# Kernel optimization log

Hardware: AMD Instinct MI355X
Metric: run time of the kernel (lower is better)

Reference implementation:

```python
import jax, jax.numpy as jnp
import numpy as np

BATCH, TAU, INPUT, HIDDEN, OUT = 131072, 20, 1, 64, 1


def setup_inputs() -> dict:
    key = jax.random.key(0)
    ks = jax.random.split(key, 8)
    fan_in = INPUT + HIDDEN
    bound = 1.0 / np.sqrt(fan_in)
    return {
        "x": jax.random.normal(ks[0], (BATCH, TAU), dtype=jnp.float32),
        "h0": jax.random.normal(ks[1], (BATCH, HIDDEN), dtype=jnp.float32),
        "Wf": jax.random.uniform(ks[2], (HIDDEN, fan_in), jnp.float32, -bound, bound),
        "bf": jax.random.uniform(ks[3], (HIDDEN,), jnp.float32, -bound, bound),
        "Wc": jax.random.uniform(ks[4], (HIDDEN, fan_in), jnp.float32, -bound, bound),
        "bc": jax.random.uniform(ks[5], (HIDDEN,), jnp.float32, -bound, bound),
        "Wo": jax.random.uniform(ks[6], (OUT, HIDDEN), jnp.float32, -1.0 / np.sqrt(HIDDEN), 1.0 / np.sqrt(HIDDEN)),
        "bo": jax.random.uniform(ks[7], (OUT,), jnp.float32, -1.0 / np.sqrt(HIDDEN), 1.0 / np.sqrt(HIDDEN)),
    }


def reference(x, h0, Wf, bf, Wc, bc, Wo, bo):
    # x: [B, tau] -> xs: [tau, B, 1], matching torch.reshape(x.T, (tau, B, 1))
    xs = jnp.transpose(x)[:, :, None]

    def step(H, X):
        inp = jnp.concatenate([X, H], axis=1)              # [B, 1+H]
        F = jax.nn.sigmoid(inp @ Wf.T + bf)                # forget gate [B, H]
        inp2 = jnp.concatenate([X, F * H], axis=1)
        H_tilda = jnp.tanh(inp2 @ Wc.T + bc)               # candidate [B, H]
        H_new = (1.0 - F) * H + F * H_tilda
        return H_new, None

    H, _ = jax.lax.scan(step, h0, xs)
    return H @ Wo.T + bo                                   # [B, 1]
```

## Files before the change

kernel.cpp:

```cpp
#include <hip/hip_runtime.h>


constexpr int BATCH = 131072;
constexpr int TAU   = 20;
constexpr int HID   = 64;
constexpr int FAN   = 65;
constexpr int NT    = 256;
constexpr int ROWS  = 64;

typedef float    f32x4 __attribute__((ext_vector_type(4)));
typedef _Float16 f16x8 __attribute__((ext_vector_type(8)));
typedef unsigned u32x4 __attribute__((ext_vector_type(4)));

static constexpr float LOG2E  = 1.4426950408889634f;
static constexpr float RCP256 = 0.00390625f;

static __device__ __forceinline__ unsigned pkrtz(float a, float b) {
    return __builtin_bit_cast(unsigned, __builtin_amdgcn_cvt_pkrtz(a, b));
}
#define PK8(a0,a1,a2,a3,a4,a5,a6,a7) \
    __builtin_bit_cast(f16x8, (u32x4){pkrtz(a0,a1), pkrtz(a2,a3), \
                                      pkrtz(a4,a5), pkrtz(a6,a7)})

#define MFMAH(A, B, C) __builtin_amdgcn_mfma_f32_16x16x32_f16((A), (B), (C), 0, 0, 0)

#define HOFF(g, T, s) ((((g) * 8) + ((T) * 2) + (s)) * 512)

#define LD_HI(g, T, s)  (*(const f16x8*)&sWhi[HOFF(g, T, s) + Lx8])
#define LD_AUG(g, T)    (*(const f16x8*)&sAug[augMul * ((g) * 4 + (T)) + augSel])

#define SIGF4(F, C) { \
    const float e0_ = __builtin_amdgcn_exp2f(C[0]); \
    const float e1_ = __builtin_amdgcn_exp2f(C[1]); \
    const float e2_ = __builtin_amdgcn_exp2f(C[2]); \
    const float e3_ = __builtin_amdgcn_exp2f(C[3]); \
    const float d0_ = 1.0f + e0_, d1_ = 1.0f + e1_; \
    const float d2_ = 1.0f + e2_, d3_ = 1.0f + e3_; \
    const float d01_ = d0_ * d1_, d23_ = d2_ * d3_; \
    const float ii_  = __builtin_amdgcn_rcpf(d01_ * d23_); \
    const float i01_ = ii_ * d23_, i23_ = ii_ * d01_; \
    F[0] = d1_ * i01_; F[1] = d0_ * i01_; \
    F[2] = d3_ * i23_; F[3] = d2_ * i23_; }

#define UPDF4(S, F, C) { \
    const float e0_ = __builtin_amdgcn_exp2f(C[0]); \
    const float e1_ = __builtin_amdgcn_exp2f(C[1]); \
    const float e2_ = __builtin_amdgcn_exp2f(C[2]); \
    const float e3_ = __builtin_amdgcn_exp2f(C[3]); \
    const float d0_ = 1.0f + e0_, d1_ = 1.0f + e1_; \
    const float d2_ = 1.0f + e2_, d3_ = 1.0f + e3_; \
    const float d01_ = d0_ * d1_, d23_ = d2_ * d3_; \
    const float ii_  = __builtin_amdgcn_rcpf(d01_ * d23_); \
    const float j01_ = -2.0f * (ii_ * d23_), j23_ = -2.0f * (ii_ * d01_); \
    const float t0_ = fmaf(d1_, j01_, 1.0f); \
    const float t1_ = fmaf(d0_, j01_, 1.0f); \
    const float t2_ = fmaf(d3_, j23_, 1.0f); \
    const float t3_ = fmaf(d2_, j23_, 1.0f); \
    S[0] = fmaf(F[0], t0_ - S[0], S[0]); S[1] = fmaf(F[1], t1_ - S[1], S[1]); \
    S[2] = fmaf(F[2], t2_ - S[2], S[2]); S[3] = fmaf(F[3], t3_ - S[3], S[3]); }

#define FTILE(T, FT) { \
    f32x4 ch_ = MFMAH(LD_AUG(0, T), augB, z4); \
    ch_ = MFMAH(LD_HI(0, T, 0), BS0, ch_); \
    ch_ = MFMAH(LD_HI(0, T, 1), BS1, ch_); \
    SIGF4(FT, ch_) }

__global__ __launch_bounds__(NT, 3) void mgu_fwd(
    const float* __restrict__ x,
    const float* __restrict__ h0,
    const float* __restrict__ Wf,
    const float* __restrict__ bfv,
    const float* __restrict__ Wc,
    const float* __restrict__ bcv,
    const float* __restrict__ Wo,
    const float* __restrict__ bov,
    float* __restrict__ out)
{
    __shared__ _Float16 sWhi[8192];
    __shared__ _Float16 sAug[1032];
    __shared__ float sX[ROWS * TAU];
    __shared__ float sWo[HID];

    const int tid = threadIdx.x;
    const long rb0 = (long)blockIdx.x * ROWS;

    for (int idx = tid; idx < 8192; idx += NT) {
        const int i = idx & 7, Li = (idx >> 3) & 63, s = (idx >> 9) & 1,
                  T = (idx >> 10) & 3, g = (idx >> 12) & 1;
        const int u = 16 * (2 * s + (i >> 2)) + 4 * (Li >> 4) + (i & 3);
        const float* Wg = g ? Wc : Wf;
        const float sc = g ? (2.0f * LOG2E) : (-LOG2E);
        sWhi[HOFF(g, T, s) + (idx & 511)] =
            (_Float16)(sc * Wg[(16 * T + (Li & 15)) * FAN + 1 + u]);
    }
    if (tid < 128) {
        const int m = tid & 15, T = (tid >> 4) & 3, g = tid >> 6;
        const float* Wg = g ? Wc : Wf;
        const float* bg = g ? bcv : bfv;
        const float sc = g ? (2.0f * LOG2E) : (-LOG2E);
        const float fx = sc * Wg[(16 * T + m) * FAN];
        const float fb = sc * bg[16 * T + m];
        const _Float16 fxh = (_Float16)fx;
        const _Float16 fbh = (_Float16)fb;
        _Float16* c = &sAug[(g * 4 + T) * 128 + m * 8];
        c[0] = fxh;
        c[1] = (_Float16)((fx - (float)fxh) * 256.0f);
        c[2] = fxh;
        c[3] = fbh;
        c[4] = (_Float16)((fb - (float)fbh) * 256.0f);
        c[5] = (_Float16)0.0f; c[6] = (_Float16)0.0f; c[7] = (_Float16)0.0f;
    }
    if (tid < 8) sAug[1024 + tid] = (_Float16)0.0f;
    for (int i2 = tid; i2 < ROWS * TAU; i2 += NT) sX[i2] = x[rb0 * TAU + i2];
    if (tid < HID) sWo[tid] = Wo[tid];
    __syncthreads();

    const int w = tid >> 6, L = tid & 63, q = L >> 4, r = L & 15;
    const int lr = w * 16 + r;
    const long gr = rb0 + lr;
    const int Lx8 = L * 8;

    const int augMul = (q == 0) ? 128 : 0;
    const int augSel = (q == 0) ? (r * 8) : 1024;

    const f32x4 z4 = {0.f, 0.f, 0.f, 0.f};

    f32x4 S0 = *(const f32x4*)&h0[gr * HID +  0 + 4 * q];
    f32x4 S1 = *(const f32x4*)&h0[gr * HID + 16 + 4 * q];
    f32x4 S2 = *(const f32x4*)&h0[gr * HID + 32 + 4 * q];
    f32x4 S3 = *(const f32x4*)&h0[gr * HID + 48 + 4 * q];

    #pragma unroll 1
    for (int t = 0; t < TAU; ++t) {
        const float xt = sX[lr * TAU + t];
        f16x8 augB;
        {
            const _Float16 xh = (_Float16)xt;
            const float xhf = (float)xh;
            unsigned d0 = pkrtz(xhf, xhf * RCP256);
            unsigned d1 = pkrtz(xt - xhf, 1.0f);
            unsigned d2 = pkrtz(RCP256, 0.0f);
            if (q != 0) { d0 = 0; d1 = 0; d2 = 0; }
            augB = __builtin_bit_cast(f16x8, (u32x4){d0, d1, d2, 0u});
        }

        const f16x8 BS0 = PK8(S0[0],S0[1],S0[2],S0[3], S1[0],S1[1],S1[2],S1[3]);
        const f16x8 BS1 = PK8(S2[0],S2[1],S2[2],S2[3], S3[0],S3[1],S3[2],S3[3]);

        f32x4 CcH0 = MFMAH(LD_AUG(1, 0), augB, z4);
        f32x4 CcH1 = MFMAH(LD_AUG(1, 1), augB, z4);
        f32x4 CcH2 = MFMAH(LD_AUG(1, 2), augB, z4);
        f32x4 CcH3 = MFMAH(LD_AUG(1, 3), augB, z4);

        f32x4 F0, F1, F2, F3;
        FTILE(0, F0)
        FTILE(1, F1)

        const f32x4 G0 = F0 * S0, G1 = F1 * S1;
        const f16x8 BG0 = PK8(G0[0],G0[1],G0[2],G0[3], G1[0],G1[1],G1[2],G1[3]);
        __builtin_amdgcn_s_setprio(1);
        CcH0 = MFMAH(LD_HI(1, 0, 0), BG0, CcH0);
        CcH1 = MFMAH(LD_HI(1, 1, 0), BG0, CcH1);
        CcH2 = MFMAH(LD_HI(1, 2, 0), BG0, CcH2);
        CcH3 = MFMAH(LD_HI(1, 3, 0), BG0, CcH3);
        __builtin_amdgcn_s_setprio(0);

        FTILE(2, F2)
        FTILE(3, F3)

        const f32x4 G2 = F2 * S2, G3 = F3 * S3;
        const f16x8 BG1 = PK8(G2[0],G2[1],G2[2],G2[3], G3[0],G3[1],G3[2],G3[3]);
        __builtin_amdgcn_s_setprio(1);
        CcH0 = MFMAH(LD_HI(1, 0, 1), BG1, CcH0);
        CcH1 = MFMAH(LD_HI(1, 1, 1), BG1, CcH1);
        CcH2 = MFMAH(LD_HI(1, 2, 1), BG1, CcH2);
        CcH3 = MFMAH(LD_HI(1, 3, 1), BG1, CcH3);
        __builtin_amdgcn_s_setprio(0);

        UPDF4(S0, F0, CcH0)
        UPDF4(S1, F1, CcH1)
        UPDF4(S2, F2, CcH2)
        UPDF4(S3, F3, CcH3)
    }

    const f32x4 wo0 = *(const f32x4*)&sWo[ 0 + 4 * q];
    const f32x4 wo1 = *(const f32x4*)&sWo[16 + 4 * q];
    const f32x4 wo2 = *(const f32x4*)&sWo[32 + 4 * q];
    const f32x4 wo3 = *(const f32x4*)&sWo[48 + 4 * q];
    float acc = 0.0f;
    acc = fmaf(wo0[0], S0[0], acc); acc = fmaf(wo0[1], S0[1], acc);
    acc = fmaf(wo0[2], S0[2], acc); acc = fmaf(wo0[3], S0[3], acc);
    acc = fmaf(wo1[0], S1[0], acc); acc = fmaf(wo1[1], S1[1], acc);
    acc = fmaf(wo1[2], S1[2], acc); acc = fmaf(wo1[3], S1[3], acc);
    acc = fmaf(wo2[0], S2[0], acc); acc = fmaf(wo2[1], S2[1], acc);
    acc = fmaf(wo2[2], S2[2], acc); acc = fmaf(wo2[3], S2[3], acc);
    acc = fmaf(wo3[0], S3[0], acc); acc = fmaf(wo3[1], S3[1], acc);
    acc = fmaf(wo3[2], S3[2], acc); acc = fmaf(wo3[3], S3[3], acc);
    acc += __shfl_xor(acc, 16, 64);
    acc += __shfl_xor(acc, 32, 64);
    if (q == 0) out[gr] = acc + bov[0];
}

extern "C" void kernel_launch(void* const* d_in, const int* in_sizes, int n_in,
                              void* d_out, int out_size, void* d_ws, size_t ws_size,
                              hipStream_t stream) {
    const float* x  = (const float*)d_in[0];
    const float* h0 = (const float*)d_in[1];
    const float* Wf = (const float*)d_in[2];
    const float* bf = (const float*)d_in[3];
    const float* Wc = (const float*)d_in[4];
    const float* bc = (const float*)d_in[5];
    const float* Wo = (const float*)d_in[6];
    const float* bo = (const float*)d_in[7];
    float* out = (float*)d_out;

    hipLaunchKernelGGL(mgu_fwd, dim3(BATCH / ROWS), dim3(NT), 0, stream,
                       x, h0, Wf, bf, Wc, bc, Wo, bo, out);
}
```

Measured before the change: 101.5 us.

## Switch recurrence matmuls to 32x32x16 MFMA with 32 batch rows per wave

```diff
diff --git a/kernel.cpp b/kernel.cpp
--- a/kernel.cpp
+++ b/kernel.cpp
@@ -6,11 +6,12 @@
 constexpr int HID   = 64;
 constexpr int FAN   = 65;
 constexpr int NT    = 256;
-constexpr int ROWS  = 64;
-
-typedef float    f32x4 __attribute__((ext_vector_type(4)));
-typedef _Float16 f16x8 __attribute__((ext_vector_type(8)));
-typedef unsigned u32x4 __attribute__((ext_vector_type(4)));
+constexpr int ROWS  = 128;
+
+typedef float    f32x4  __attribute__((ext_vector_type(4)));
+typedef float    f32x16 __attribute__((ext_vector_type(16)));
+typedef _Float16 f16x8  __attribute__((ext_vector_type(8)));
+typedef unsigned u32x4  __attribute__((ext_vector_type(4)));
 
 static constexpr float LOG2E  = 1.4426950408889634f;
 static constexpr float RCP256 = 0.00390625f;
@@ -22,31 +23,32 @@
     __builtin_bit_cast(f16x8, (u32x4){pkrtz(a0,a1), pkrtz(a2,a3), \
                                       pkrtz(a4,a5), pkrtz(a6,a7)})
 
-#define MFMAH(A, B, C) __builtin_amdgcn_mfma_f32_16x16x32_f16((A), (B), (C), 0, 0, 0)
-
-#define HOFF(g, T, s) ((((g) * 8) + ((T) * 2) + (s)) * 512)
-
-#define LD_HI(g, T, s)  (*(const f16x8*)&sWhi[HOFF(g, T, s) + Lx8])
-#define LD_AUG(g, T)    (*(const f16x8*)&sAug[augMul * ((g) * 4 + (T)) + augSel])
-
-#define SIGF4(F, C) { \
-    const float e0_ = __builtin_amdgcn_exp2f(C[0]); \
-    const float e1_ = __builtin_amdgcn_exp2f(C[1]); \
-    const float e2_ = __builtin_amdgcn_exp2f(C[2]); \
-    const float e3_ = __builtin_amdgcn_exp2f(C[3]); \
+#define MFMA32(A, B, C) __builtin_amdgcn_mfma_f32_32x32x16_f16((A), (B), (C), 0, 0, 0)
+
+#define WOFF(g, M, s) (((((g) * 2) + (M)) * 4 + (s)) * 512)
+#define AOFF(g, M) ((((g) * 2) + (M)) * 512)
+
+#define LD_W(g, M, s) (*(const f16x8*)&sWhi[WOFF(g, M, s) + Lx8])
+#define LD_AUG(g, M)  (*(const f16x8*)&sAug[AOFF(g, M) + Lx8])
+
+#define SIGQ(F, C, q) { \
+    const float e0_ = __builtin_amdgcn_exp2f(C[4*(q)+0]); \
+    const float e1_ = __builtin_amdgcn_exp2f(C[4*(q)+1]); \
+    const float e2_ = __builtin_amdgcn_exp2f(C[4*(q)+2]); \
+    const float e3_ = __builtin_amdgcn_exp2f(C[4*(q)+3]); \
     const float d0_ = 1.0f + e0_, d1_ = 1.0f + e1_; \
     const float d2_ = 1.0f + e2_, d3_ = 1.0f + e3_; \
     const float d01_ = d0_ * d1_, d23_ = d2_ * d3_; \
     const float ii_  = __builtin_amdgcn_rcpf(d01_ * d23_); \
     const float i01_ = ii_ * d23_, i23_ = ii_ * d01_; \
-    F[0] = d1_ * i01_; F[1] = d0_ * i01_; \
-    F[2] = d3_ * i23_; F[3] = d2_ * i23_; }
-
-#define UPDF4(S, F, C) { \
-    const float e0_ = __builtin_amdgcn_exp2f(C[0]); \
-    const float e1_ = __builtin_amdgcn_exp2f(C[1]); \
-    const float e2_ = __builtin_amdgcn_exp2f(C[2]); \
-    const float e3_ = __builtin_amdgcn_exp2f(C[3]); \
+    F[4*(q)+0] = d1_ * i01_; F[4*(q)+1] = d0_ * i01_; \
+    F[4*(q)+2] = d3_ * i23_; F[4*(q)+3] = d2_ * i23_; }
+
+#define UPDQ(S, F, C, q) { \
+    const float e0_ = __builtin_amdgcn_exp2f(C[4*(q)+0]); \
+    const float e1_ = __builtin_amdgcn_exp2f(C[4*(q)+1]); \
+    const float e2_ = __builtin_amdgcn_exp2f(C[4*(q)+2]); \
+    const float e3_ = __builtin_amdgcn_exp2f(C[4*(q)+3]); \
     const float d0_ = 1.0f + e0_, d1_ = 1.0f + e1_; \
     const float d2_ = 1.0f + e2_, d3_ = 1.0f + e3_; \
     const float d01_ = d0_ * d1_, d23_ = d2_ * d3_; \
@@ -56,16 +58,25 @@
     const float t1_ = fmaf(d0_, j01_, 1.0f); \
     const float t2_ = fmaf(d3_, j23_, 1.0f); \
     const float t3_ = fmaf(d2_, j23_, 1.0f); \
-    S[0] = fmaf(F[0], t0_ - S[0], S[0]); S[1] = fmaf(F[1], t1_ - S[1], S[1]); \
-    S[2] = fmaf(F[2], t2_ - S[2], S[2]); S[3] = fmaf(F[3], t3_ - S[3], S[3]); }
-
-#define FTILE(T, FT) { \
-    f32x4 ch_ = MFMAH(LD_AUG(0, T), augB, z4); \
-    ch_ = MFMAH(LD_HI(0, T, 0), BS0, ch_); \
-    ch_ = MFMAH(LD_HI(0, T, 1), BS1, ch_); \
-    SIGF4(FT, ch_) }
-
-__global__ __launch_bounds__(NT, 3) void mgu_fwd(
+    S[4*(q)+0] = fmaf(F[4*(q)+0], t0_ - S[4*(q)+0], S[4*(q)+0]); \
+    S[4*(q)+1] = fmaf(F[4*(q)+1], t1_ - S[4*(q)+1], S[4*(q)+1]); \
+    S[4*(q)+2] = fmaf(F[4*(q)+2], t2_ - S[4*(q)+2], S[4*(q)+2]); \
+    S[4*(q)+3] = fmaf(F[4*(q)+3], t3_ - S[4*(q)+3], S[4*(q)+3]); }
+
+#define FGATE(M, F) { \
+    f32x16 cf_ = MFMA32(LD_AUG(0, M), augB, z16); \
+    cf_ = MFMA32(LD_W(0, M, 0), BS0, cf_); \
+    cf_ = MFMA32(LD_W(0, M, 1), BS1, cf_); \
+    cf_ = MFMA32(LD_W(0, M, 2), BS2, cf_); \
+    cf_ = MFMA32(LD_W(0, M, 3), BS3, cf_); \
+    SIGQ(F, cf_, 0) SIGQ(F, cf_, 1) SIGQ(F, cf_, 2) SIGQ(F, cf_, 3) }
+
+#define BGS(s) PK8(F0[4*(s)+0]*S0[4*(s)+0], F0[4*(s)+1]*S0[4*(s)+1], \
+                   F0[4*(s)+2]*S0[4*(s)+2], F0[4*(s)+3]*S0[4*(s)+3], \
+                   F1[4*(s)+0]*S1[4*(s)+0], F1[4*(s)+1]*S1[4*(s)+1], \
+                   F1[4*(s)+2]*S1[4*(s)+2], F1[4*(s)+3]*S1[4*(s)+3])
+
+__global__ __launch_bounds__(NT, 2) void mgu_fwd(
     const float* __restrict__ x,
     const float* __restrict__ h0,
     const float* __restrict__ Wf,
@@ -77,7 +88,7 @@
     float* __restrict__ out)
 {
     __shared__ _Float16 sWhi[8192];
-    __shared__ _Float16 sAug[1032];
+    __shared__ _Float16 sAug[2048];
     __shared__ float sX[ROWS * TAU];
     __shared__ float sWo[HID];
 
@@ -85,54 +96,64 @@
     const long rb0 = (long)blockIdx.x * ROWS;
 
     for (int idx = tid; idx < 8192; idx += NT) {
-        const int i = idx & 7, Li = (idx >> 3) & 63, s = (idx >> 9) & 1,
-                  T = (idx >> 10) & 3, g = (idx >> 12) & 1;
-        const int u = 16 * (2 * s + (i >> 2)) + 4 * (Li >> 4) + (i & 3);
+        const int c = idx >> 9, p = idx & 511;
+        const int Lr = p >> 3, i = p & 7;
+        const int g = c >> 3, M = (c >> 2) & 1, s = c & 3;
+        const int m = 32 * M + (Lr & 31);
+        const int u = (i & 3) + 4 * (Lr >> 5) + 8 * s + 32 * (i >> 2);
         const float* Wg = g ? Wc : Wf;
         const float sc = g ? (2.0f * LOG2E) : (-LOG2E);
-        sWhi[HOFF(g, T, s) + (idx & 511)] =
-            (_Float16)(sc * Wg[(16 * T + (Li & 15)) * FAN + 1 + u]);
-    }
-    if (tid < 128) {
-        const int m = tid & 15, T = (tid >> 4) & 3, g = tid >> 6;
-        const float* Wg = g ? Wc : Wf;
-        const float* bg = g ? bcv : bfv;
-        const float sc = g ? (2.0f * LOG2E) : (-LOG2E);
-        const float fx = sc * Wg[(16 * T + m) * FAN];
-        const float fb = sc * bg[16 * T + m];
-        const _Float16 fxh = (_Float16)fx;
-        const _Float16 fbh = (_Float16)fb;
-        _Float16* c = &sAug[(g * 4 + T) * 128 + m * 8];
-        c[0] = fxh;
-        c[1] = (_Float16)((fx - (float)fxh) * 256.0f);
-        c[2] = fxh;
-        c[3] = fbh;
-        c[4] = (_Float16)((fb - (float)fbh) * 256.0f);
-        c[5] = (_Float16)0.0f; c[6] = (_Float16)0.0f; c[7] = (_Float16)0.0f;
-    }
-    if (tid < 8) sAug[1024 + tid] = (_Float16)0.0f;
+        sWhi[idx] = (_Float16)(sc * Wg[m * FAN + 1 + u]);
+    }
+    for (int idx = tid; idx < 2048; idx += NT) {
+        const int c = idx >> 9, p = idx & 511;
+        const int Lr = p >> 3, i = p & 7;
+        const int g = c >> 1, M = c & 1;
+        _Float16 v = (_Float16)0.0f;
+        if (Lr < 32 && i < 5) {
+            const float* Wg = g ? Wc : Wf;
+            const float* bg = g ? bcv : bfv;
+            const float sc = g ? (2.0f * LOG2E) : (-LOG2E);
+            const int m = 32 * M + Lr;
+            const float fx = sc * Wg[m * FAN];
+            const float fb = sc * bg[m];
+            const float fxh = (float)(_Float16)fx;
+            const float fbh = (float)(_Float16)fb;
+            v = (i == 0) ? (_Float16)fx
+              : (i == 1) ? (_Float16)((fx - fxh) * 256.0f)
+              : (i == 2) ? (_Float16)fx
+              : (i == 3) ? (_Float16)fb
+              :            (_Float16)((fb - fbh) * 256.0f);
+        }
+        sAug[idx] = v;
+    }
     for (int i2 = tid; i2 < ROWS * TAU; i2 += NT) sX[i2] = x[rb0 * TAU + i2];
     if (tid < HID) sWo[tid] = Wo[tid];
     __syncthreads();
 
-    const int w = tid >> 6, L = tid & 63, q = L >> 4, r = L & 15;
-    const int lr = w * 16 + r;
-    const long gr = rb0 + lr;
+    const int w = tid >> 6, L = tid & 63;
+    const int hh = L >> 5;
+    const int n  = L & 31;
+    const int lrow = w * 32 + n;
+    const long gr = rb0 + lrow;
     const int Lx8 = L * 8;
 
-    const int augMul = (q == 0) ? 128 : 0;
-    const int augSel = (q == 0) ? (r * 8) : 1024;
-
-    const f32x4 z4 = {0.f, 0.f, 0.f, 0.f};
-
-    f32x4 S0 = *(const f32x4*)&h0[gr * HID +  0 + 4 * q];
-    f32x4 S1 = *(const f32x4*)&h0[gr * HID + 16 + 4 * q];
-    f32x4 S2 = *(const f32x4*)&h0[gr * HID + 32 + 4 * q];
-    f32x4 S3 = *(const f32x4*)&h0[gr * HID + 48 + 4 * q];
+    const f32x16 z16 = {0.f,0.f,0.f,0.f,0.f,0.f,0.f,0.f,
+                        0.f,0.f,0.f,0.f,0.f,0.f,0.f,0.f};
+
+    f32x16 S0, S1;
+    {
+        const float* hp = h0 + gr * HID + 4 * hh;
+#define LDQ(SM, M, q) { const f32x4 v_ = *(const f32x4*)(hp + 32*(M) + 8*(q)); \
+        SM[4*(q)+0]=v_[0]; SM[4*(q)+1]=v_[1]; SM[4*(q)+2]=v_[2]; SM[4*(q)+3]=v_[3]; }
+        LDQ(S0,0,0) LDQ(S0,0,1) LDQ(S0,0,2) LDQ(S0,0,3)
+        LDQ(S1,1,0) LDQ(S1,1,1) LDQ(S1,1,2) LDQ(S1,1,3)
+#undef LDQ
+    }
 
     #pragma unroll 1
     for (int t = 0; t < TAU; ++t) {
-        const float xt = sX[lr * TAU + t];
+        const float xt = sX[lrow * TAU + t];
         f16x8 augB;
         {
             const _Float16 xh = (_Float16)xt;
@@ -140,65 +161,48 @@
             unsigned d0 = pkrtz(xhf, xhf * RCP256);
             unsigned d1 = pkrtz(xt - xhf, 1.0f);
             unsigned d2 = pkrtz(RCP256, 0.0f);
-            if (q != 0) { d0 = 0; d1 = 0; d2 = 0; }
+            if (hh != 0) { d0 = 0; d1 = 0; d2 = 0; }
             augB = __builtin_bit_cast(f16x8, (u32x4){d0, d1, d2, 0u});
         }
 
-        const f16x8 BS0 = PK8(S0[0],S0[1],S0[2],S0[3], S1[0],S1[1],S1[2],S1[3]);
-        const f16x8 BS1 = PK8(S2[0],S2[1],S2[2],S2[3], S3[0],S3[1],S3[2],S3[3]);
-
-        f32x4 CcH0 = MFMAH(LD_AUG(1, 0), augB, z4);
-        f32x4 CcH1 = MFMAH(LD_AUG(1, 1), augB, z4);
-        f32x4 CcH2 = MFMAH(LD_AUG(1, 2), augB, z4);
-        f32x4 CcH3 = MFMAH(LD_AUG(1, 3), augB, z4);
-
-        f32x4 F0, F1, F2, F3;
-        FTILE(0, F0)
-        FTILE(1, F1)
-
-        const f32x4 G0 = F0 * S0, G1 = F1 * S1;
-        const f16x8 BG0 = PK8(G0[0],G0[1],G0[2],G0[3], G1[0],G1[1],G1[2],G1[3]);
+        const f16x8 BS0 = PK8(S0[ 0],S0[ 1],S0[ 2],S0[ 3], S1[ 0],S1[ 1],S1[ 2],S1[ 3]);
+        const f16x8 BS1 = PK8(S0[ 4],S0[ 5],S0[ 6],S0[ 7], S1[ 4],S1[ 5],S1[ 6],S1[ 7]);
+        const f16x8 BS2 = PK8(S0[ 8],S0[ 9],S0[10],S0[11], S1[ 8],S1[ 9],S1[10],S1[11]);
+        const f16x8 BS3 = PK8(S0[12],S0[13],S0[14],S0[15], S1[12],S1[13],S1[14],S1[15]);
+
+        f32x16 F0, F1;
+        FGATE(0, F0)
+        FGATE(1, F1)
+
+        f32x16 Cc0 = MFMA32(LD_AUG(1, 0), augB, z16);
+        f32x16 Cc1 = MFMA32(LD_AUG(1, 1), augB, z16);
         __builtin_amdgcn_s_setprio(1);
-        CcH0 = MFMAH(LD_HI(1, 0, 0), BG0, CcH0);
-        CcH1 = MFMAH(LD_HI(1, 1, 0), BG0, CcH1);
-        CcH2 = MFMAH(LD_HI(1, 2, 0), BG0, CcH2);
-        CcH3 = MFMAH(LD_HI(1, 3, 0), BG0, CcH3);
+        { const f16x8 bg_ = BGS(0);
+          Cc0 = MFMA32(LD_W(1, 0, 0), bg_, Cc0); Cc1 = MFMA32(LD_W(1, 1, 0), bg_, Cc1); }
+        { const f16x8 bg_ = BGS(1);
+          Cc0 = MFMA32(LD_W(1, 0, 1), bg_, Cc0); Cc1 = MFMA32(LD_W(1, 1, 1), bg_, Cc1); }
+        { const f16x8 bg_ = BGS(2);
+          Cc0 = MFMA32(LD_W(1, 0, 2), bg_, Cc0); Cc1 = MFMA32(LD_W(1, 1, 2), bg_, Cc1); }
+        { const f16x8 bg_ = BGS(3);
+          Cc0 = MFMA32(LD_W(1, 0, 3), bg_, Cc0); Cc1 = MFMA32(LD_W(1, 1, 3), bg_, Cc1); }
         __builtin_amdgcn_s_setprio(0);
 
-        FTILE(2, F2)
-        FTILE(3, F3)
-
-        const f32x4 G2 = F2 * S2, G3 = F3 * S3;
-        const f16x8 BG1 = PK8(G2[0],G2[1],G2[2],G2[3], G3[0],G3[1],G3[2],G3[3]);
-        __builtin_amdgcn_s_setprio(1);
-        CcH0 = MFMAH(LD_HI(1, 0, 1), BG1, CcH0);
-        CcH1 = MFMAH(LD_HI(1, 1, 1), BG1, CcH1);
-        CcH2 = MFMAH(LD_HI(1, 2, 1), BG1, CcH2);
-        CcH3 = MFMAH(LD_HI(1, 3, 1), BG1, CcH3);
-        __builtin_amdgcn_s_setprio(0);
-
-        UPDF4(S0, F0, CcH0)
-        UPDF4(S1, F1, CcH1)
-        UPDF4(S2, F2, CcH2)
-        UPDF4(S3, F3, CcH3)
-    }
-
-    const f32x4 wo0 = *(const f32x4*)&sWo[ 0 + 4 * q];
-    const f32x4 wo1 = *(const f32x4*)&sWo[16 + 4 * q];
-    const f32x4 wo2 = *(const f32x4*)&sWo[32 + 4 * q];
-    const f32x4 wo3 = *(const f32x4*)&sWo[48 + 4 * q];
+        UPDQ(S0, F0, Cc0, 0) UPDQ(S0, F0, Cc0, 1)
+        UPDQ(S0, F0, Cc0, 2) UPDQ(S0, F0, Cc0, 3)
+        UPDQ(S1, F1, Cc1, 0) UPDQ(S1, F1, Cc1, 1)
+        UPDQ(S1, F1, Cc1, 2) UPDQ(S1, F1, Cc1, 3)
+    }
+
     float acc = 0.0f;
-    acc = fmaf(wo0[0], S0[0], acc); acc = fmaf(wo0[1], S0[1], acc);
-    acc = fmaf(wo0[2], S0[2], acc); acc = fmaf(wo0[3], S0[3], acc);
-    acc = fmaf(wo1[0], S1[0], acc); acc = fmaf(wo1[1], S1[1], acc);
-    acc = fmaf(wo1[2], S1[2], acc); acc = fmaf(wo1[3], S1[3], acc);
-    acc = fmaf(wo2[0], S2[0], acc); acc = fmaf(wo2[1], S2[1], acc);
-    acc = fmaf(wo2[2], S2[2], acc); acc = fmaf(wo2[3], S2[3], acc);
-    acc = fmaf(wo3[0], S3[0], acc); acc = fmaf(wo3[1], S3[1], acc);
-    acc = fmaf(wo3[2], S3[2], acc); acc = fmaf(wo3[3], S3[3], acc);
-    acc += __shfl_xor(acc, 16, 64);
+#define WOACC(SM, M, q) { \
+    const f32x4 wv_ = *(const f32x4*)&sWo[32*(M) + 8*(q) + 4*hh]; \
+    acc = fmaf(wv_[0], SM[4*(q)+0], acc); acc = fmaf(wv_[1], SM[4*(q)+1], acc); \
+    acc = fmaf(wv_[2], SM[4*(q)+2], acc); acc = fmaf(wv_[3], SM[4*(q)+3], acc); }
+    WOACC(S0, 0, 0) WOACC(S0, 0, 1) WOACC(S0, 0, 2) WOACC(S0, 0, 3)
+    WOACC(S1, 1, 0) WOACC(S1, 1, 1) WOACC(S1, 1, 2) WOACC(S1, 1, 3)
+#undef WOACC
     acc += __shfl_xor(acc, 32, 64);
-    if (q == 0) out[gr] = acc + bov[0];
+    if (L < 32) out[gr] = acc + bov[0];
 }
 
 extern "C" void kernel_launch(void* const* d_in, const int* in_sizes, int n_in,
```

Measured after the change: 101.4 us. Within noise of the previous version (-0.2%).

## Drop x staging in LDS, prefetch x per step, reorder MFMA schedule for occupancy

Applied to the files above, without the earlier changes.

```diff
diff --git a/kernel.cpp b/kernel.cpp
--- a/kernel.cpp
+++ b/kernel.cpp
@@ -59,13 +59,7 @@
     S[0] = fmaf(F[0], t0_ - S[0], S[0]); S[1] = fmaf(F[1], t1_ - S[1], S[1]); \
     S[2] = fmaf(F[2], t2_ - S[2], S[2]); S[3] = fmaf(F[3], t3_ - S[3], S[3]); }
 
-#define FTILE(T, FT) { \
-    f32x4 ch_ = MFMAH(LD_AUG(0, T), augB, z4); \
-    ch_ = MFMAH(LD_HI(0, T, 0), BS0, ch_); \
-    ch_ = MFMAH(LD_HI(0, T, 1), BS1, ch_); \
-    SIGF4(FT, ch_) }
-
-__global__ __launch_bounds__(NT, 3) void mgu_fwd(
+__global__ __launch_bounds__(NT, 4) void mgu_fwd(
     const float* __restrict__ x,
     const float* __restrict__ h0,
     const float* __restrict__ Wf,
@@ -78,7 +72,6 @@
 {
     __shared__ _Float16 sWhi[8192];
     __shared__ _Float16 sAug[1032];
-    __shared__ float sX[ROWS * TAU];
     __shared__ float sWo[HID];
 
     const int tid = threadIdx.x;
@@ -111,13 +104,11 @@
         c[5] = (_Float16)0.0f; c[6] = (_Float16)0.0f; c[7] = (_Float16)0.0f;
     }
     if (tid < 8) sAug[1024 + tid] = (_Float16)0.0f;
-    for (int i2 = tid; i2 < ROWS * TAU; i2 += NT) sX[i2] = x[rb0 * TAU + i2];
     if (tid < HID) sWo[tid] = Wo[tid];
     __syncthreads();
 
     const int w = tid >> 6, L = tid & 63, q = L >> 4, r = L & 15;
-    const int lr = w * 16 + r;
-    const long gr = rb0 + lr;
+    const long gr = rb0 + (w * 16 + r);
     const int Lx8 = L * 8;
 
     const int augMul = (q == 0) ? 128 : 0;
@@ -130,9 +121,13 @@
     f32x4 S2 = *(const f32x4*)&h0[gr * HID + 32 + 4 * q];
     f32x4 S3 = *(const f32x4*)&h0[gr * HID + 48 + 4 * q];
 
+    const float* xr = x + gr * TAU;
+    float xt = xr[0];
+
     #pragma unroll 1
     for (int t = 0; t < TAU; ++t) {
-        const float xt = sX[lr * TAU + t];
+        const float xn = (t + 1 < TAU) ? xr[t + 1] : 0.0f;
+
         f16x8 augB;
         {
             const _Float16 xh = (_Float16)xt;
@@ -144,43 +139,57 @@
             augB = __builtin_bit_cast(f16x8, (u32x4){d0, d1, d2, 0u});
         }
 
-        const f16x8 BS0 = PK8(S0[0],S0[1],S0[2],S0[3], S1[0],S1[1],S1[2],S1[3]);
-        const f16x8 BS1 = PK8(S2[0],S2[1],S2[2],S2[3], S3[0],S3[1],S3[2],S3[3]);
-
-        f32x4 CcH0 = MFMAH(LD_AUG(1, 0), augB, z4);
-        f32x4 CcH1 = MFMAH(LD_AUG(1, 1), augB, z4);
-        f32x4 CcH2 = MFMAH(LD_AUG(1, 2), augB, z4);
-        f32x4 CcH3 = MFMAH(LD_AUG(1, 3), augB, z4);
+        f32x4 Cf0 = MFMAH(LD_AUG(0, 0), augB, z4);
+        f32x4 Cf1 = MFMAH(LD_AUG(0, 1), augB, z4);
+        f32x4 Cf2 = MFMAH(LD_AUG(0, 2), augB, z4);
+        f32x4 Cf3 = MFMAH(LD_AUG(0, 3), augB, z4);
+        {
+            const f16x8 BS0 = PK8(S0[0],S0[1],S0[2],S0[3], S1[0],S1[1],S1[2],S1[3]);
+            Cf0 = MFMAH(LD_HI(0, 0, 0), BS0, Cf0);
+            Cf1 = MFMAH(LD_HI(0, 1, 0), BS0, Cf1);
+            Cf2 = MFMAH(LD_HI(0, 2, 0), BS0, Cf2);
+            Cf3 = MFMAH(LD_HI(0, 3, 0), BS0, Cf3);
+        }
+        {
+            const f16x8 BS1 = PK8(S2[0],S2[1],S2[2],S2[3], S3[0],S3[1],S3[2],S3[3]);
+            Cf0 = MFMAH(LD_HI(0, 0, 1), BS1, Cf0);
+            Cf1 = MFMAH(LD_HI(0, 1, 1), BS1, Cf1);
+            Cf2 = MFMAH(LD_HI(0, 2, 1), BS1, Cf2);
+            Cf3 = MFMAH(LD_HI(0, 3, 1), BS1, Cf3);
+        }
 
         f32x4 F0, F1, F2, F3;
-        FTILE(0, F0)
-        FTILE(1, F1)
-
-        const f32x4 G0 = F0 * S0, G1 = F1 * S1;
-        const f16x8 BG0 = PK8(G0[0],G0[1],G0[2],G0[3], G1[0],G1[1],G1[2],G1[3]);
+        SIGF4(F0, Cf0) SIGF4(F1, Cf1) SIGF4(F2, Cf2) SIGF4(F3, Cf3)
+
+        f32x4 Cc0 = MFMAH(LD_AUG(1, 0), augB, z4);
+        f32x4 Cc1 = MFMAH(LD_AUG(1, 1), augB, z4);
+        f32x4 Cc2 = MFMAH(LD_AUG(1, 2), augB, z4);
+        f32x4 Cc3 = MFMAH(LD_AUG(1, 3), augB, z4);
         __builtin_amdgcn_s_setprio(1);
-        CcH0 = MFMAH(LD_HI(1, 0, 0), BG0, CcH0);
-        CcH1 = MFMAH(LD_HI(1, 1, 0), BG0, CcH1);
-        CcH2 = MFMAH(LD_HI(1, 2, 0), BG0, CcH2);
-        CcH3 = MFMAH(LD_HI(1, 3, 0), BG0, CcH3);
+        {
+            const f16x8 BG0 = PK8(F0[0]*S0[0], F0[1]*S0[1], F0[2]*S0[2], F0[3]*S0[3],
+                                  F1[0]*S1[0], F1[1]*S1[1], F1[2]*S1[2], F1[3]*S1[3]);
+            Cc0 = MFMAH(LD_HI(1, 0, 0), BG0, Cc0);
+            Cc1 = MFMAH(LD_HI(1, 1, 0), BG0, Cc1);
+            Cc2 = MFMAH(LD_HI(1, 2, 0), BG0, Cc2);
+            Cc3 = MFMAH(LD_HI(1, 3, 0), BG0, Cc3);
+        }
+        {
+            const f16x8 BG1 = PK8(F2[0]*S2[0], F2[1]*S2[1], F2[2]*S2[2], F2[3]*S2[3],
+                                  F3[0]*S3[0], F3[1]*S3[1], F3[2]*S3[2], F3[3]*S3[3]);
+            Cc0 = MFMAH(LD_HI(1, 0, 1), BG1, Cc0);
+            Cc1 = MFMAH(LD_HI(1, 1, 1), BG1, Cc1);
+            Cc2 = MFMAH(LD_HI(1, 2, 1), BG1, Cc2);
+            Cc3 = MFMAH(LD_HI(1, 3, 1), BG1, Cc3);
+        }
         __builtin_amdgcn_s_setprio(0);
 
-        FTILE(2, F2)
-        FTILE(3, F3)
-
-        const f32x4 G2 = F2 * S2, G3 = F3 * S3;
-        const f16x8 BG1 = PK8(G2[0],G2[1],G2[2],G2[3], G3[0],G3[1],G3[2],G3[3]);
-        __builtin_amdgcn_s_setprio(1);
-        CcH0 = MFMAH(LD_HI(1, 0, 1), BG1, CcH0);
-        CcH1 = MFMAH(LD_HI(1, 1, 1), BG1, CcH1);
-        CcH2 = MFMAH(LD_HI(1, 2, 1), BG1, CcH2);
-        CcH3 = MFMAH(LD_HI(1, 3, 1), BG1, CcH3);
-        __builtin_amdgcn_s_setprio(0);
-
-        UPDF4(S0, F0, CcH0)
-        UPDF4(S1, F1, CcH1)
-        UPDF4(S2, F2, CcH2)
-        UPDF4(S3, F3, CcH3)
+        UPDF4(S0, F0, Cc0)
+        UPDF4(S1, F1, Cc1)
+        UPDF4(S2, F2, Cc2)
+        UPDF4(S3, F3, Cc3)
+
+        xt = xn;
     }
 
     const f32x4 wo0 = *(const f32x4*)&sWo[ 0 + 4 * q];
```

Measured after the change: 188.0 us. +85.2%, slower.
